# Optimization experiments

Measured on AMD Instinct MI355X. Metric: run time of the kernel, lower is better.

The kernel has to match this reference:

```python
import jax, jax.numpy as jnp
import numpy as np

B, C, H, W = 64, 128, 32, 32
GROUPS = 32
EPS = 1e-6
SCALE = 0.044194173824159216  # 1/sqrt(512), as hardcoded in the torch module


def setup_inputs() -> dict:
    key = jax.random.key(0)
    ks = jax.random.split(key, 12)
    s = 1.0 / np.sqrt(C)
    return {
        "x": jax.random.normal(ks[0], (B, C, H, W), dtype=jnp.float32),
        "gn_w": jax.random.normal(ks[1], (C,), dtype=jnp.float32) * 0.02 + 1.0,
        "gn_b": jax.random.normal(ks[2], (C,), dtype=jnp.float32) * 0.02,
        "wq": jax.random.uniform(ks[3], (C, C), jnp.float32, -s, s),
        "bq": jax.random.uniform(ks[4], (C,), jnp.float32, -s, s),
        "wk": jax.random.uniform(ks[5], (C, C), jnp.float32, -s, s),
        "bk": jax.random.uniform(ks[6], (C,), jnp.float32, -s, s),
        "wv": jax.random.uniform(ks[7], (C, C), jnp.float32, -s, s),
        "bv": jax.random.uniform(ks[8], (C,), jnp.float32, -s, s),
        "wo": jax.random.uniform(ks[9], (C, C), jnp.float32, -s, s),
        "bo": jax.random.uniform(ks[10], (C,), jnp.float32, -s, s),
    }


def reference(x, gn_w, gn_b, wq, bq, wk, bk, wv, bv, wo, bo):
    b = x.shape[0]
    res = x
    # GroupNorm(32 groups, 128 channels): normalize over (channels_per_group, H, W)
    xg = x.reshape(b, GROUPS, C // GROUPS, H * W)
    mean = xg.mean(axis=(2, 3), keepdims=True)
    var = xg.var(axis=(2, 3), keepdims=True)
    xn = (xg - mean) * jax.lax.rsqrt(var + EPS)
    xn = xn.reshape(b, C, H, W) * gn_w[:, None, None] + gn_b[:, None, None]
    # flatten spatial -> sequence: [b, S=1024, C=128]
    t = xn.reshape(b, C, H * W).transpose(0, 2, 1)
    q = t @ wq.T + bq
    k = t @ wk.T + bk
    v = t @ wv.T + bv
    att = jnp.einsum('bsc,btc->bst', q, k) * SCALE  # [b, S, S]
    att = jax.nn.softmax(att, axis=-1)
    o = jnp.einsum('bst,btc->bsc', att, v)
    o = o @ wo.T + bo
    out = o.transpose(0, 2, 1).reshape(b, C, H, W) + res
    return out
```

## Files before the change

### kernel.cpp

```cpp
#include <hip/hip_runtime.h>
#include <hip/hip_bf16.h>

#define BATCH 64
#define CCH 128
#define SEQ 1024
#define NG 32
#define EPSV 1e-6f
#define SCALEV 0.044194173824159216f
#define QPRE (0.044194173824159216f * 1.4426950408889634f)

typedef short v8s __attribute__((ext_vector_type(8)));
typedef short v4s __attribute__((ext_vector_type(4)));
typedef float v4f __attribute__((ext_vector_type(4)));
typedef int   v4i __attribute__((ext_vector_type(4)));
typedef unsigned short us;

__device__ __forceinline__ us f2bf(float f) {
    __hip_bfloat16 h = __float2bfloat16(f);
    return *reinterpret_cast<us*>(&h);
}

__device__ __forceinline__ int cvtpk(float lo, float hi) {
    int r;
    asm("v_cvt_pk_bf16_f32 %0, %1, %2" : "=v"(r) : "v"(lo), "v"(hi));
    return r;
}

#if __has_builtin(__builtin_amdgcn_exp2f)
#define EXP2F(x) __builtin_amdgcn_exp2f(x)
#else
#define EXP2F(x) exp2f(x)
#endif

#define MFMA16(a, b, c) __builtin_amdgcn_mfma_f32_16x16x32_bf16(a, b, c, 0, 0, 0)

__device__ __forceinline__ void gld_lds16(const us* g, us* l) {
    __builtin_amdgcn_global_load_lds(
        (const __attribute__((address_space(1))) void*)g,
        (__attribute__((address_space(3))) void*)l, 16, 0, 0);
}

__global__ void prep_gn(const float* __restrict__ wq, const float* __restrict__ wk,
                        const float* __restrict__ wv, const float* __restrict__ wo,
                        us* wbf, const float* __restrict__ x,
                        float* meanr, float* rstdr) {
    int tid = threadIdx.x;
    if (blockIdx.x < 256) {
        int i = blockIdx.x * 256 + tid;
        const float* srcs[4] = {wq, wk, wv, wo};
        wbf[i] = f2bf(srcs[i >> 14][i & 16383]);
        return;
    }
    int bg = blockIdx.x - 256;
    const float4* p = (const float4*)(x + (size_t)bg * (4 * SEQ));
    float s1 = 0.f, s2 = 0.f;
    #pragma unroll
    for (int i = 0; i < 4; i++) {
        float4 v = p[i * 256 + tid];
        s1 += v.x + v.y + v.z + v.w;
        s2 += v.x * v.x + v.y * v.y + v.z * v.z + v.w * v.w;
    }
    #pragma unroll
    for (int off = 32; off; off >>= 1) {
        s1 += __shfl_down(s1, off);
        s2 += __shfl_down(s2, off);
    }
    __shared__ float a1[4], a2[4];
    int w = tid >> 6, l = tid & 63;
    if (l == 0) { a1[w] = s1; a2[w] = s2; }
    __syncthreads();
    if (tid == 0) {
        float t1 = a1[0] + a1[1] + a1[2] + a1[3];
        float t2 = a2[0] + a2[1] + a2[2] + a2[3];
        float mean = t1 * (1.0f / (4 * SEQ));
        float var  = t2 * (1.0f / (4 * SEQ)) - mean * mean;
        meanr[bg] = mean;
        rstdr[bg] = rsqrtf(var + EPSV);
    }
}

__global__ __launch_bounds__(256, 2) void qkv_kernel(
    const float* __restrict__ x, const float* __restrict__ gn_w,
    const float* __restrict__ gn_b, const float* __restrict__ meanr,
    const float* __restrict__ rstdr, const us* __restrict__ wbf,
    const float* __restrict__ bq, const float* __restrict__ bk,
    const float* __restrict__ bv,
    us* Q, us* K, us* Vt)
{
    __shared__ us tls[64 * 136];
    __shared__ float sa[CCH], sb[CCH];
    int b  = blockIdx.x >> 4;
    int s0 = (blockIdx.x & 15) * 64;
    int tid = threadIdx.x;
    const float* xb = x + (size_t)b * CCH * SEQ;

    if (tid < CCH) {
        int g = tid >> 2;
        float rs = rstdr[b * NG + g];
        float mu = meanr[b * NG + g];
        float a_ = rs * gn_w[tid];
        sa[tid] = a_;
        sb[tid] = gn_b[tid] - mu * a_;
    }
    __syncthreads();

    #pragma unroll
    for (int rep = 0; rep < 8; rep++) {
        int idx = rep * 256 + tid;
        int c = idx >> 4, s4 = idx & 15;
        float4 v = *(const float4*)&xb[c * SEQ + s0 + s4 * 4];
        float a_ = sa[c], b_ = sb[c];
        int sbase = s4 * 4;
        tls[(sbase + 0) * 136 + c] = f2bf(v.x * a_ + b_);
        tls[(sbase + 1) * 136 + c] = f2bf(v.y * a_ + b_);
        tls[(sbase + 2) * 136 + c] = f2bf(v.z * a_ + b_);
        tls[(sbase + 3) * 136 + c] = f2bf(v.w * a_ + b_);
    }
    __syncthreads();

    int w = tid >> 6, lane = tid & 63;
    int m = lane & 15, quad = lane >> 4;

    v8s bfr[6][4];
    float bias[6];
    #pragma unroll
    for (int t = 0; t < 6; t++) {
        int T = w * 6 + t;
        int o = T >> 3, ct = T & 7;
        const us* wmat = wbf + o * 16384;
        #pragma unroll
        for (int ch = 0; ch < 4; ch++)
            bfr[t][ch] = *(const v8s*)&wmat[(ct * 16 + m) * 128 + ch * 32 + quad * 8];
        const float* bb = (o == 0) ? bq : (o == 1) ? bk : bv;
        bias[t] = bb[ct * 16 + m];
    }

    us* Qb = Q + (size_t)b * SEQ * CCH;
    us* Kb = K + (size_t)b * SEQ * CCH;
    us* Vb = Vt + (size_t)b * CCH * SEQ;

    #pragma unroll
    for (int st = 0; st < 4; st++) {
        v8s a[4];
        #pragma unroll
        for (int ch = 0; ch < 4; ch++)
            a[ch] = *(const v8s*)&tls[(st * 16 + m) * 136 + ch * 32 + quad * 8];
        int srow = s0 + st * 16 + quad * 4;
        #pragma unroll
        for (int t = 0; t < 6; t++) {
            int T = w * 6 + t;
            int o = T >> 3, ct = T & 7;
            v4f acc = {0,0,0,0};
            #pragma unroll
            for (int ch = 0; ch < 4; ch++)
                acc = MFMA16(a[ch], bfr[t][ch], acc);
            int col = ct * 16 + m;
            if (o == 0) {
                #pragma unroll
                for (int r = 0; r < 4; r++)
                    Qb[(size_t)(srow + r) * 128 + col] = f2bf((acc[r] + bias[t]) * QPRE);
            } else if (o == 1) {
                #pragma unroll
                for (int r = 0; r < 4; r++)
                    Kb[(size_t)(srow + r) * 128 + col] = f2bf(acc[r] + bias[t]);
            } else {
                v4s pk;
                #pragma unroll
                for (int r = 0; r < 4; r++) pk[r] = (short)f2bf(acc[r] + bias[t]);
                *(v4s*)&Vb[(size_t)col * SEQ + srow] = pk;
            }
        }
    }
}

__global__ __launch_bounds__(256, 2) void attn_kernel(
    const us* __restrict__ Q, const us* __restrict__ K,
    const us* __restrict__ Vt, const us* __restrict__ wbo,
    const float* __restrict__ bo, const float* __restrict__ x,
    float* __restrict__ out)
{
    __shared__ char smem_raw[65536];

    int i = blockIdx.x;
    int b  = (i & 7) * 8 + ((i >> 3) & 7);
    int qt = i >> 6;
    int tid = threadIdx.x;
    int w = tid >> 6, lane = tid & 63;
    int m = lane & 15, quad = lane >> 4;
    int qrow0 = qt * 128 + w * 32;
    const us* Qb = Q + (size_t)b * SEQ * CCH;
    const us* Kb = K + (size_t)b * SEQ * CCH;
    const us* Vb = Vt + (size_t)b * CCH * SEQ;

    v8s aq[2][4];
    #pragma unroll
    for (int st = 0; st < 2; st++)
        #pragma unroll
        for (int ch = 0; ch < 4; ch++)
            aq[st][ch] = *(const v8s*)&Qb[(size_t)(qrow0 + st * 16 + m) * 128 + ch * 32 + quad * 8];

    v4f oacc[2][8];
    #pragma unroll
    for (int st = 0; st < 2; st++)
        #pragma unroll
        for (int ct = 0; ct < 8; ct++) oacc[st][ct] = (v4f){0, 0, 0, 0};
    float lrun[2] = {0.f, 0.f};

    const us* kg[4]; const us* vg[4];
    int jb = w * 4;
    #pragma unroll
    for (int j4 = 0; j4 < 4; j4++) {
        int j = jb + j4;
        int kr = 4 * j + (lane >> 4);
        kg[j4] = Kb + (size_t)kr * 128 + ((lane & 15) ^ (kr & 15)) * 8;
        int vc = 8 * j + (lane >> 3);
        vg[j4] = Vb + (size_t)vc * SEQ + ((lane & 7) ^ (vc & 7)) * 8;
    }
    int idx0 = 2 * (quad & 1) * 16 + m;
    int idx1 = idx0 + 16;

    #pragma unroll
    for (int j4 = 0; j4 < 4; j4++) {
        gld_lds16(kg[j4], (us*)smem_raw + (jb + j4) * 512);
        gld_lds16(vg[j4], (us*)(smem_raw + 16384) + (jb + j4) * 512);
    }

    for (int kt = 0; kt < 16; kt++) {
        int boff  = (kt & 1) ? 32768 : 0;
        int boffn = boff ^ 32768;
        __builtin_amdgcn_s_barrier();
        if (kt < 15) {
            #pragma unroll
            for (int j4 = 0; j4 < 4; j4++) {
                gld_lds16(kg[j4] + (size_t)(kt + 1) * 8192,
                          (us*)(smem_raw + boffn) + (jb + j4) * 512);
                gld_lds16(vg[j4] + (size_t)(kt + 1) * 64,
                          (us*)(smem_raw + boffn + 16384) + (jb + j4) * 512);
            }
            asm volatile("s_waitcnt vmcnt(8)" ::: "memory");
        } else {
            asm volatile("s_waitcnt vmcnt(0)" ::: "memory");
        }
        __builtin_amdgcn_s_barrier();

        const us* kl = (const us*)(smem_raw + boff);
        const us* vl = (const us*)(smem_raw + boff + 16384);

        v4f acc0[4], acc1[4];
        __builtin_amdgcn_s_setprio(1);
        #pragma unroll
        for (int c2 = 0; c2 < 4; c2++) {
            int krow = c2 * 16 + m;
            acc0[c2] = (v4f){0, 0, 0, 0};
            acc1[c2] = (v4f){0, 0, 0, 0};
            #pragma unroll
            for (int ch = 0; ch < 4; ch++) {
                int chunk = (ch * 4 + quad) ^ (krow & 15);
                v8s kb = *(const v8s*)&kl[krow * 128 + chunk * 8];
                acc0[c2] = MFMA16(kb, aq[0][ch], acc0[c2]);
                acc1[c2] = MFMA16(kb, aq[1][ch], acc1[c2]);
            }
        }
        __builtin_amdgcn_s_setprio(0);

        int e[2][4][2];
        #pragma unroll
        for (int c2 = 0; c2 < 4; c2++) {
            float p0[4], p1[4];
            #pragma unroll
            for (int r = 0; r < 4; r++) {
                p0[r] = EXP2F(acc0[c2][r]);
                p1[r] = EXP2F(acc1[c2][r]);
                lrun[0] += p0[r];
                lrun[1] += p1[r];
            }
            e[0][c2][0] = cvtpk(p0[0], p0[1]);
            e[0][c2][1] = cvtpk(p0[2], p0[3]);
            e[1][c2][0] = cvtpk(p1[0], p1[1]);
            e[1][c2][1] = cvtpk(p1[2], p1[3]);
        }
        v8s pa[2][2];
        #pragma unroll
        for (int st = 0; st < 2; st++)
            #pragma unroll
            for (int kc2 = 0; kc2 < 2; kc2++) {
                int c0 = (quad < 2) ? e[st][2 * kc2][0] : e[st][2 * kc2 + 1][0];
                int c1 = (quad < 2) ? e[st][2 * kc2][1] : e[st][2 * kc2 + 1][1];
                v4i t;
                t[0] = __shfl(c0, idx0);
                t[1] = __shfl(c1, idx0);
                t[2] = __shfl(c0, idx1);
                t[3] = __shfl(c1, idx1);
                pa[st][kc2] = __builtin_bit_cast(v8s, t);
            }
        __builtin_amdgcn_s_setprio(1);
        #pragma unroll
        for (int ct = 0; ct < 8; ct++) {
            int vrow = ct * 16 + m;
            #pragma unroll
            for (int kc2 = 0; kc2 < 2; kc2++) {
                int chunk = (kc2 * 4 + quad) ^ (vrow & 7);
                v8s vb = *(const v8s*)&vl[vrow * 64 + chunk * 8];
                oacc[0][ct] = MFMA16(pa[0][kc2], vb, oacc[0][ct]);
                oacc[1][ct] = MFMA16(pa[1][kc2], vb, oacc[1][ct]);
            }
        }
        __builtin_amdgcn_s_setprio(0);
    }

    float inv[2][4];
    #pragma unroll
    for (int st = 0; st < 2; st++) {
        float rs = lrun[st];
        rs += __shfl_xor(rs, 16);
        rs += __shfl_xor(rs, 32);
        #pragma unroll
        for (int r = 0; r < 4; r++)
            inv[st][r] = 1.0f / __shfl(rs, quad * 4 + r);
    }
    __syncthreads();
    us* olds = (us*)smem_raw;
    #pragma unroll
    for (int st = 0; st < 2; st++)
        #pragma unroll
        for (int ct = 0; ct < 8; ct++)
            #pragma unroll
            for (int r = 0; r < 4; r++)
                olds[(w * 32 + st * 16 + quad * 4 + r) * 136 + ct * 16 + m] =
                    f2bf(oacc[st][ct][r] * inv[st][r]);
    __syncthreads();

    const float* xb = x + (size_t)b * CCH * SEQ;
    float* ob = out + (size_t)b * CCH * SEQ;
    int sbase = qt * 128 + w * 32;
    v8s obf[2][4];
    #pragma unroll
    for (int st = 0; st < 2; st++)
        #pragma unroll
        for (int ch = 0; ch < 4; ch++)
            obf[st][ch] = *(const v8s*)&olds[(w * 32 + st * 16 + m) * 136 + ch * 32 + quad * 8];
    #pragma unroll
    for (int mt = 0; mt < 8; mt++) {
        v8s af[4];
        #pragma unroll
        for (int ch = 0; ch < 4; ch++)
            af[ch] = *(const v8s*)&wbo[(mt * 16 + m) * 128 + ch * 32 + quad * 8];
        #pragma unroll
        for (int st = 0; st < 2; st++) {
            v4f acc = {0,0,0,0};
            #pragma unroll
            for (int ch = 0; ch < 4; ch++)
                acc = MFMA16(af[ch], obf[st][ch], acc);
            #pragma unroll
            for (int r = 0; r < 4; r++) {
                int c = mt * 16 + quad * 4 + r;
                int idx = c * SEQ + sbase + st * 16 + m;
                ob[idx] = acc[r] + bo[c] + xb[idx];
            }
        }
    }
}

extern "C" void kernel_launch(void* const* d_in, const int* in_sizes, int n_in,
                              void* d_out, int out_size, void* d_ws, size_t ws_size,
                              hipStream_t stream) {
    const float* x    = (const float*)d_in[0];
    const float* gn_w = (const float*)d_in[1];
    const float* gn_b = (const float*)d_in[2];
    const float* wq   = (const float*)d_in[3];
    const float* bq   = (const float*)d_in[4];
    const float* wk   = (const float*)d_in[5];
    const float* bk   = (const float*)d_in[6];
    const float* wv   = (const float*)d_in[7];
    const float* bv   = (const float*)d_in[8];
    const float* wo   = (const float*)d_in[9];
    const float* bo   = (const float*)d_in[10];
    float* out = (float*)d_out;

    char* ws = (char*)d_ws;
    us* wbf      = (us*)ws;
    float* meanr = (float*)(ws + 131072);
    float* rstdr = (float*)(ws + 139264);
    us* Qbuf     = (us*)(ws + 147456);
    us* Kbuf     = (us*)(ws + 147456 + 16777216ull);
    us* Vtbuf    = (us*)(ws + 147456 + 2ull * 16777216ull);

    prep_gn<<<256 + BATCH * NG, 256, 0, stream>>>(wq, wk, wv, wo, wbf, x, meanr, rstdr);
    qkv_kernel<<<1024, 256, 0, stream>>>(x, gn_w, gn_b, meanr, rstdr, wbf,
                                         bq, bk, bv, Qbuf, Kbuf, Vtbuf);
    attn_kernel<<<512, 256, 0, stream>>>(Qbuf, Kbuf, Vtbuf, wbf + 3 * 16384,
                                         bo, x, out);
}
```

Measured before the change: 171.7 us.

## Interleave QK MFMA with exp and split PV by k-chunk; raise qkv occupancy

In the attention kernel, the QK^T MFMA steps are interleaved with the exp2/pack work of the previous column block, and the PV product is split into two halves so the shuffle of the second half can overlap the MFMAs of the first. The aim is to hide transcendental and cross-lane latency behind matrix-core work. The QKV kernel now keeps the activation tile in registers and loops over weight tiles one at a time, which lowers register pressure so launch bounds can request 4 blocks per CU instead of 2. This relies on the compiler keeping the intended instruction order, and the higher occupancy target may cause spills.

```diff
diff --git a/kernel.cpp b/kernel.cpp
--- a/kernel.cpp
+++ b/kernel.cpp
@@ -79,7 +79,7 @@
     }
 }
 
-__global__ __launch_bounds__(256, 2) void qkv_kernel(
+__global__ __launch_bounds__(256, 4) void qkv_kernel(
     const float* __restrict__ x, const float* __restrict__ gn_w,
     const float* __restrict__ gn_b, const float* __restrict__ meanr,
     const float* __restrict__ rstdr, const us* __restrict__ wbf,
@@ -121,52 +121,49 @@
     int w = tid >> 6, lane = tid & 63;
     int m = lane & 15, quad = lane >> 4;
 
-    v8s bfr[6][4];
-    float bias[6];
+    v8s a[4][4];
+    #pragma unroll
+    for (int st = 0; st < 4; st++)
+        #pragma unroll
+        for (int ch = 0; ch < 4; ch++)
+            a[st][ch] = *(const v8s*)&tls[(st * 16 + m) * 136 + ch * 32 + quad * 8];
+
+    us* Qb = Q + (size_t)b * SEQ * CCH;
+    us* Kb = K + (size_t)b * SEQ * CCH;
+    us* Vb = Vt + (size_t)b * CCH * SEQ;
+
     #pragma unroll
     for (int t = 0; t < 6; t++) {
         int T = w * 6 + t;
         int o = T >> 3, ct = T & 7;
+        int col = ct * 16 + m;
         const us* wmat = wbf + o * 16384;
+        v8s bfr[4];
         #pragma unroll
         for (int ch = 0; ch < 4; ch++)
-            bfr[t][ch] = *(const v8s*)&wmat[(ct * 16 + m) * 128 + ch * 32 + quad * 8];
+            bfr[ch] = *(const v8s*)&wmat[(ct * 16 + m) * 128 + ch * 32 + quad * 8];
         const float* bb = (o == 0) ? bq : (o == 1) ? bk : bv;
-        bias[t] = bb[ct * 16 + m];
-    }
-
-    us* Qb = Q + (size_t)b * SEQ * CCH;
-    us* Kb = K + (size_t)b * SEQ * CCH;
-    us* Vb = Vt + (size_t)b * CCH * SEQ;
-
-    #pragma unroll
-    for (int st = 0; st < 4; st++) {
-        v8s a[4];
-        #pragma unroll
-        for (int ch = 0; ch < 4; ch++)
-            a[ch] = *(const v8s*)&tls[(st * 16 + m) * 136 + ch * 32 + quad * 8];
-        int srow = s0 + st * 16 + quad * 4;
-        #pragma unroll
-        for (int t = 0; t < 6; t++) {
-            int T = w * 6 + t;
-            int o = T >> 3, ct = T & 7;
+        float bias = bb[col];
+
+        #pragma unroll
+        for (int st = 0; st < 4; st++) {
             v4f acc = {0,0,0,0};
             #pragma unroll
             for (int ch = 0; ch < 4; ch++)
-                acc = MFMA16(a[ch], bfr[t][ch], acc);
-            int col = ct * 16 + m;
+                acc = MFMA16(a[st][ch], bfr[ch], acc);
+            int srow = s0 + st * 16 + quad * 4;
             if (o == 0) {
                 #pragma unroll
                 for (int r = 0; r < 4; r++)
-                    Qb[(size_t)(srow + r) * 128 + col] = f2bf((acc[r] + bias[t]) * QPRE);
+                    Qb[(size_t)(srow + r) * 128 + col] = f2bf((acc[r] + bias) * QPRE);
             } else if (o == 1) {
                 #pragma unroll
                 for (int r = 0; r < 4; r++)
-                    Kb[(size_t)(srow + r) * 128 + col] = f2bf(acc[r] + bias[t]);
+                    Kb[(size_t)(srow + r) * 128 + col] = f2bf(acc[r] + bias);
             } else {
                 v4s pk;
                 #pragma unroll
-                for (int r = 0; r < 4; r++) pk[r] = (short)f2bf(acc[r] + bias[t]);
+                for (int r = 0; r < 4; r++) pk[r] = (short)f2bf(acc[r] + bias);
                 *(v4s*)&Vb[(size_t)col * SEQ + srow] = pk;
             }
         }
@@ -246,66 +243,78 @@
         const us* kl = (const us*)(smem_raw + boff);
         const us* vl = (const us*)(smem_raw + boff + 16384);
 
+        __builtin_amdgcn_s_setprio(1);
+
         v4f acc0[4], acc1[4];
-        __builtin_amdgcn_s_setprio(1);
-        #pragma unroll
-        for (int c2 = 0; c2 < 4; c2++) {
-            int krow = c2 * 16 + m;
-            acc0[c2] = (v4f){0, 0, 0, 0};
-            acc1[c2] = (v4f){0, 0, 0, 0};
-            #pragma unroll
-            for (int ch = 0; ch < 4; ch++) {
-                int chunk = (ch * 4 + quad) ^ (krow & 15);
-                v8s kb = *(const v8s*)&kl[krow * 128 + chunk * 8];
-                acc0[c2] = MFMA16(kb, aq[0][ch], acc0[c2]);
-                acc1[c2] = MFMA16(kb, aq[1][ch], acc1[c2]);
-            }
+        int e[2][4][2];
+
+        #define QK_STEP(c2) { \
+            int krow = (c2) * 16 + m; \
+            v4f A0 = {0,0,0,0}, A1 = {0,0,0,0}; \
+            _Pragma("unroll") \
+            for (int ch = 0; ch < 4; ch++) { \
+                int chunk = (ch * 4 + quad) ^ (krow & 15); \
+                v8s kb = *(const v8s*)&kl[krow * 128 + chunk * 8]; \
+                A0 = MFMA16(kb, aq[0][ch], A0); \
+                A1 = MFMA16(kb, aq[1][ch], A1); \
+            } \
+            acc0[c2] = A0; acc1[c2] = A1; }
+
+        #define EXP_STEP(c2) { \
+            float p0[4], p1[4]; \
+            _Pragma("unroll") \
+            for (int r = 0; r < 4; r++) { \
+                p0[r] = EXP2F(acc0[c2][r]); \
+                p1[r] = EXP2F(acc1[c2][r]); \
+                lrun[0] += p0[r]; lrun[1] += p1[r]; \
+            } \
+            e[0][c2][0] = cvtpk(p0[0], p0[1]); e[0][c2][1] = cvtpk(p0[2], p0[3]); \
+            e[1][c2][0] = cvtpk(p1[0], p1[1]); e[1][c2][1] = cvtpk(p1[2], p1[3]); }
+
+        QK_STEP(0)
+        QK_STEP(1)
+        EXP_STEP(0)
+        QK_STEP(2)
+        EXP_STEP(1)
+        QK_STEP(3)
+        EXP_STEP(2)
+        EXP_STEP(3)
+
+        #define SHFL_STEP(kc2, paw) { \
+            _Pragma("unroll") \
+            for (int st = 0; st < 2; st++) { \
+                int c0 = (quad < 2) ? e[st][2 * (kc2)][0] : e[st][2 * (kc2) + 1][0]; \
+                int c1 = (quad < 2) ? e[st][2 * (kc2)][1] : e[st][2 * (kc2) + 1][1]; \
+                v4i t; \
+                t[0] = __shfl(c0, idx0); \
+                t[1] = __shfl(c1, idx0); \
+                t[2] = __shfl(c0, idx1); \
+                t[3] = __shfl(c1, idx1); \
+                paw[st] = __builtin_bit_cast(v8s, t); } }
+
+        v8s pa0[2], pa1[2];
+        SHFL_STEP(0, pa0)
+        #pragma unroll
+        for (int ct = 0; ct < 8; ct++) {
+            int vrow = ct * 16 + m;
+            int chunk = quad ^ (vrow & 7);
+            v8s vb = *(const v8s*)&vl[vrow * 64 + chunk * 8];
+            oacc[0][ct] = MFMA16(pa0[0], vb, oacc[0][ct]);
+            oacc[1][ct] = MFMA16(pa0[1], vb, oacc[1][ct]);
+        }
+        SHFL_STEP(1, pa1)
+        #pragma unroll
+        for (int ct = 0; ct < 8; ct++) {
+            int vrow = ct * 16 + m;
+            int chunk = (4 + quad) ^ (vrow & 7);
+            v8s vb = *(const v8s*)&vl[vrow * 64 + chunk * 8];
+            oacc[0][ct] = MFMA16(pa1[0], vb, oacc[0][ct]);
+            oacc[1][ct] = MFMA16(pa1[1], vb, oacc[1][ct]);
         }
         __builtin_amdgcn_s_setprio(0);
-
-        int e[2][4][2];
-        #pragma unroll
-        for (int c2 = 0; c2 < 4; c2++) {
-            float p0[4], p1[4];
-            #pragma unroll
-            for (int r = 0; r < 4; r++) {
-                p0[r] = EXP2F(acc0[c2][r]);
-                p1[r] = EXP2F(acc1[c2][r]);
-                lrun[0] += p0[r];
-                lrun[1] += p1[r];
-            }
-            e[0][c2][0] = cvtpk(p0[0], p0[1]);
-            e[0][c2][1] = cvtpk(p0[2], p0[3]);
-            e[1][c2][0] = cvtpk(p1[0], p1[1]);
-            e[1][c2][1] = cvtpk(p1[2], p1[3]);
-        }
-        v8s pa[2][2];
-        #pragma unroll
-        for (int st = 0; st < 2; st++)
-            #pragma unroll
-            for (int kc2 = 0; kc2 < 2; kc2++) {
-                int c0 = (quad < 2) ? e[st][2 * kc2][0] : e[st][2 * kc2 + 1][0];
-                int c1 = (quad < 2) ? e[st][2 * kc2][1] : e[st][2 * kc2 + 1][1];
-                v4i t;
-                t[0] = __shfl(c0, idx0);
-                t[1] = __shfl(c1, idx0);
-                t[2] = __shfl(c0, idx1);
-                t[3] = __shfl(c1, idx1);
-                pa[st][kc2] = __builtin_bit_cast(v8s, t);
-            }
-        __builtin_amdgcn_s_setprio(1);
-        #pragma unroll
-        for (int ct = 0; ct < 8; ct++) {
-            int vrow = ct * 16 + m;
-            #pragma unroll
-            for (int kc2 = 0; kc2 < 2; kc2++) {
-                int chunk = (kc2 * 4 + quad) ^ (vrow & 7);
-                v8s vb = *(const v8s*)&vl[vrow * 64 + chunk * 8];
-                oacc[0][ct] = MFMA16(pa[0][kc2], vb, oacc[0][ct]);
-                oacc[1][ct] = MFMA16(pa[1][kc2], vb, oacc[1][ct]);
-            }
-        }
-        __builtin_amdgcn_s_setprio(0);
+        #undef QK_STEP
+        #undef EXP_STEP
+        #undef SHFL_STEP
     }
 
     float inv[2][4];
```

After: 168.1 us. 1.02x faster.
